# Optimization experiments

Hardware: AMD Instinct MI355X
Metric: run time of the kernel (lower is better)

## Reference

```python
import jax, jax.numpy as jnp
import numpy as np

DIM = 1024
NHEADS = 16
DIM_HEAD = 64
HIDDEN = NHEADS * DIM_HEAD  # 1024


def _xavier(key, fan_in, fan_out):
    limit = np.sqrt(6.0 / (fan_in + fan_out))
    return jax.random.uniform(key, (fan_in, fan_out), jnp.float32, -limit, limit)


def setup_inputs() -> dict:
    key = jax.random.key(0)
    kq, k1, k2, k3 = jax.random.split(key, 4)
    q = jax.random.normal(kq, (2, 2048, DIM), jnp.float32)
    Wq = _xavier(k1, DIM, HIDDEN)
    bq = jnp.zeros((HIDDEN,), jnp.float32)
    Wkv = _xavier(k2, DIM, 2 * HIDDEN)
    bkv = jnp.zeros((2 * HIDDEN,), jnp.float32)
    Wo = _xavier(k3, HIDDEN, DIM)
    bo = jnp.zeros((DIM,), jnp.float32)
    return {"q": q, "Wq": Wq, "bq": bq, "Wkv": Wkv, "bkv": bkv, "Wo": Wo, "bo": bo}


def reference(q, Wq, bq, Wkv, bkv, Wo, bo):
    scale = DIM_HEAD ** (-0.5)
    query = q @ Wq + bq                      # [b, s, hidden]
    kv = q @ Wkv + bkv                       # self-attention: kv from q
    key_, value = jnp.split(kv, 2, axis=-1)  # [b, s, hidden] each
    b, s, _ = query.shape
    query = query.reshape(b, s, NHEADS, DIM_HEAD)
    key_ = key_.reshape(b, s, NHEADS, DIM_HEAD)
    value = value.reshape(b, s, NHEADS, DIM_HEAD)
    scores = jnp.einsum('bqhd,bkhd->bhqk', query, key_) * scale
    attn = jax.nn.softmax(scores, axis=-1)
    out = jnp.einsum('bhqk,bkhd->bqhd', attn, value)
    out = out.reshape(b, s, HIDDEN)
    return out @ Wo + bo
```

## Files before the change

### kernel.cpp

```cpp
#include <hip/hip_runtime.h>

#define DIM 1024
#define NHEADS 16
#define DH 64
#define BATCH 2
#define SEQ 2048

typedef float f32x4 __attribute__((ext_vector_type(4)));
typedef short s16x8 __attribute__((ext_vector_type(8)));
typedef short s16x4 __attribute__((ext_vector_type(4)));

__device__ __forceinline__ short f2bf(float f) {
    union { float f; unsigned u; } v; v.f = f;
    unsigned r = v.u + 0x7fffu + ((v.u >> 16) & 1u);
    return (short)(r >> 16);
}

#if defined(__has_builtin)
#if __has_builtin(__builtin_amdgcn_cvt_pk_bf16_f32)
#define HAVE_PK_BF16 1
#endif
#endif
__device__ __forceinline__ unsigned f2bf_pk(float a, float b) {
#ifdef HAVE_PK_BF16
    typedef __bf16 bf16x2_t __attribute__((ext_vector_type(2)));
    bf16x2_t r = __builtin_amdgcn_cvt_pk_bf16_f32(a, b);
    return __builtin_bit_cast(unsigned, r);
#else
    return ((unsigned)(unsigned short)f2bf(b) << 16) | (unsigned short)f2bf(a);
#endif
}
__device__ __forceinline__ s16x4 pk4(float a, float b, float c, float d) {
    union { unsigned u[2]; s16x4 v; } x;
    x.u[0] = f2bf_pk(a, b); x.u[1] = f2bf_pk(c, d);
    return x.v;
}

#if defined(__has_builtin)
#if __has_builtin(__builtin_amdgcn_exp2f)
#define EXP2(x) __builtin_amdgcn_exp2f(x)
#endif
#endif
#ifndef EXP2
#define EXP2(x) exp2f(x)
#endif

#if defined(__has_builtin)
#if __has_builtin(__builtin_amdgcn_mfma_f32_16x16x16bf16_1k)
#define MFMA16(a, b, c) __builtin_amdgcn_mfma_f32_16x16x16bf16_1k(a, b, c, 0, 0, 0)
#elif __has_builtin(__builtin_amdgcn_mfma_f32_16x16x16_bf16)
#define MFMA16(a, b, c) __builtin_amdgcn_mfma_f32_16x16x16_bf16(a, b, c, 0, 0, 0)
#endif
#endif
#ifndef MFMA16
__device__ __forceinline__ f32x4 mfma16_asm(s16x4 a, s16x4 b, f32x4 c) {
    f32x4 d;
    asm volatile("v_mfma_f32_16x16x16_bf16 %0, %1, %2, %3"
                 : "=v"(d) : "v"(a), "v"(b), "0"(c));
    return d;
}
#define MFMA16(a, b, c) mfma16_asm(a, b, c)
#endif

__device__ __forceinline__ void gld16(const void* g, void* l) {
    __builtin_amdgcn_global_load_lds(
        (const __attribute__((address_space(1))) void*)g,
        (__attribute__((address_space(3))) void*)l, 16, 0, 0);
}

__global__ __launch_bounds__(256) void preproc_kernel(
    const float* __restrict__ q, short* __restrict__ qb,
    const float* __restrict__ Wq, const float* __restrict__ Wkv,
    const float* __restrict__ Wo, short* __restrict__ WT)
{
    const int bid = blockIdx.x;
    const int t = threadIdx.x;
    if (bid < 2048) {
        const int i = (bid * 256 + t) * 8;
        float4 a = *(const float4*)(q + i);
        float4 b = *(const float4*)(q + i + 4);
        union { unsigned u[4]; s16x8 v; } o;
        o.u[0] = f2bf_pk(a.x, a.y); o.u[1] = f2bf_pk(a.z, a.w);
        o.u[2] = f2bf_pk(b.x, b.y); o.u[3] = f2bf_pk(b.z, b.w);
        *(s16x8*)(qb + i) = o.v;
    } else {
        const int tb = bid - 2048;
        const int ng = (tb & 63) * 64 + (t & 63);
        const int k0 = ((tb >> 6) * 4 + (t >> 6)) * 8;
        const float* W; int n, N;
        if (ng < 1024)      { W = Wq;  n = ng;        N = 1024; }
        else if (ng < 3072) { W = Wkv; n = ng - 1024; N = 2048; }
        else                { W = Wo;  n = ng - 3072; N = 1024; }
        float v[8];
#pragma unroll
        for (int j = 0; j < 8; ++j) v[j] = W[(size_t)(k0 + j) * N + n];
        union { unsigned u[4]; s16x8 s; } o;
        o.u[0] = f2bf_pk(v[0], v[1]); o.u[1] = f2bf_pk(v[2], v[3]);
        o.u[2] = f2bf_pk(v[4], v[5]); o.u[3] = f2bf_pk(v[6], v[7]);
        *(s16x8*)&WT[(size_t)ng * 1024 + k0] = o.s;
    }
}

template<int TM, bool OUT_BF16>
__global__ __launch_bounds__(256) void gemm_mfma_kernel(
    const short* __restrict__ A, const short* __restrict__ Bt,
    const float* __restrict__ bias0, const float* __restrict__ bias1, int nsplit,
    float s0, float s1, void* __restrict__ C, short* __restrict__ VtG, int vt_split,
    int M, int N)
{
    const int K = 1024;
    constexpr int NI = (TM == 128) ? 4 : 2;
    __shared__ short As[TM * 32];
    __shared__ short Bs[128 * 32];

    const int t    = threadIdx.x;
    const int wave = t >> 6;
    const int lane = t & 63;
    const int col  = lane & 15;
    const int quad = lane >> 4;
    const int m0 = blockIdx.y * TM;
    const int n0 = blockIdx.x * 128;
    const int wroff = (TM == 128) ? (wave >> 1) * 64 : 0;
    const int wcoff = (TM == 128) ? (wave & 1) * 64 : wave * 32;

    f32x4 acc[4][NI];
#pragma unroll
    for (int mi = 0; mi < 4; ++mi)
#pragma unroll
        for (int ni = 0; ni < NI; ++ni) acc[mi][ni] = (f32x4){0.f, 0.f, 0.f, 0.f};

    constexpr int RPW = TM / 4;
    const int ldrowA = wave * RPW + (lane >> 2);
    const int ldrowB = wave * 32  + (lane >> 2);
    const int ldcol  = (lane & 3) * 8;
    const short* Ag = A  + (size_t)(m0 + ldrowA) * K + ldcol;
    const short* Bg = Bt + (size_t)(n0 + ldrowB) * K + ldcol;
    short* AsW = &As[wave * RPW * 32];
    short* BsW = &Bs[wave * 1024];

    for (int k0 = 0; k0 < K; k0 += 32) {
        __syncthreads();
        gld16(Ag + k0, AsW);
        if (TM == 128) gld16(Ag + 16 * K + k0, AsW + 512);
        gld16(Bg + k0,          BsW);
        gld16(Bg + 16 * K + k0, BsW + 512);
        __syncthreads();

        s16x8 aA[4], bB[NI];
#pragma unroll
        for (int mi = 0; mi < 4; ++mi)
            aA[mi] = *(const s16x8*)&As[(wroff + 16 * mi + col) * 32 + quad * 8];
#pragma unroll
        for (int ni = 0; ni < NI; ++ni)
            bB[ni] = *(const s16x8*)&Bs[(wcoff + 16 * ni + col) * 32 + quad * 8];
#pragma unroll
        for (int mi = 0; mi < 4; ++mi)
#pragma unroll
            for (int ni = 0; ni < NI; ++ni)
                acc[mi][ni] = __builtin_amdgcn_mfma_f32_16x16x32_bf16(aA[mi], bB[ni], acc[mi][ni], 0, 0, 0);
    }

    float bias_v[NI], scale_v[NI];
#pragma unroll
    for (int ni = 0; ni < NI; ++ni) {
        int nb = n0 + wcoff + 16 * ni + col;
        bias_v[ni]  = (nb < nsplit) ? bias0[nb] : bias1[nb - nsplit];
        scale_v[ni] = (nb < nsplit) ? s0 : s1;
    }

    if (vt_split >= 0 && n0 >= vt_split) {
#pragma unroll
        for (int mi = 0; mi < 4; ++mi)
#pragma unroll
            for (int ni = 0; ni < NI; ++ni) {
                const int gm = m0 + wroff + 16 * mi + quad * 4;
                const int gn = n0 + wcoff + 16 * ni + col;
                const int hv = (gn - vt_split) >> 6;
                const int dv = (gn - vt_split) & 63;
                const int bb = gm >> 11, tok = gm & 2047;
                f32x4 v;
#pragma unroll
                for (int r = 0; r < 4; ++r) v[r] = (acc[mi][ni][r] + bias_v[ni]) * scale_v[ni];
                *(s16x4*)(VtG + (size_t)((bb * NHEADS + hv) * 64 + dv) * SEQ + tok) =
                    pk4(v[0], v[1], v[2], v[3]);
            }
    } else {
#pragma unroll
        for (int mi = 0; mi < 4; ++mi)
#pragma unroll
            for (int ni = 0; ni < NI; ++ni)
#pragma unroll
                for (int r = 0; r < 4; ++r) {
                    const int gm = m0 + wroff + 16 * mi + quad * 4 + r;
                    const int gn = n0 + wcoff + 16 * ni + col;
                    float v = (acc[mi][ni][r] + bias_v[ni]) * scale_v[ni];
                    if (OUT_BF16) ((short*)C)[(size_t)gm * N + gn] = f2bf(v);
                    else          ((float*)C)[(size_t)gm * N + gn] = v;
                }
    }
}

__global__ __launch_bounds__(512) void attn_v7_kernel(
    const short* __restrict__ QKV,
    const short* __restrict__ VtG,
    short* __restrict__ O)
{
    const int qt = blockIdx.x;
    const int h  = blockIdx.y;
    const int b  = blockIdx.z;
    const int t  = threadIdx.x;
    const int wave = t >> 6;
    const int lane = t & 63;
    const int col  = lane & 15;
    const int quad = lane >> 4;
    const int wq = wave & 3;
    const int kh = wave >> 2;

    __shared__ short smem[4 * 64 * 72];

    const short* Qg = QKV + (size_t)(b * SEQ + qt * 256) * 3072 + h * DH;
    const short* Kg = QKV + (size_t)(b * SEQ) * 3072 + 1024 + h * DH;
    const short* VtRow = VtG + (size_t)(b * NHEADS + h) * 64 * SEQ;

    s16x8 aQ[4][2];
#pragma unroll
    for (int tq = 0; tq < 4; ++tq)
#pragma unroll
        for (int kq = 0; kq < 2; ++kq)
            aQ[tq][kq] = *(const s16x8*)(Qg + (size_t)(wq * 64 + 16 * tq + col) * 3072 + kq * 32 + quad * 8);

    f32x4 oa[4][4];
    float lsum[4] = {0.f, 0.f, 0.f, 0.f};
#pragma unroll
    for (int td = 0; td < 4; ++td)
#pragma unroll
        for (int tq = 0; tq < 4; ++tq) oa[td][tq] = (f32x4){0.f, 0.f, 0.f, 0.f};

    const int srow = t >> 3;
    const int sc8  = (t & 7) * 8;
    const short* KgS  = Kg + (size_t)srow * 3072 + sc8;
    const short* VtgS = VtRow + (size_t)srow * SEQ + sc8;
    s16x8 kx = *(const s16x8*)KgS;
    s16x8 vx = *(const s16x8*)VtgS;

    for (int kt = 0; kt < SEQ / 64; ++kt) {
        const int curK = (kt & 1) * 4608;
        const int curV = 9216 + (kt & 1) * 4608;
        *(s16x8*)&smem[curK + srow * 72 + sc8] = kx;
        *(s16x8*)&smem[curV + srow * 72 + sc8] = vx;
        {
            int nt = (kt + 1 < SEQ / 64) ? kt + 1 : kt;
            kx = *(const s16x8*)(KgS + (size_t)nt * 64 * 3072);
            vx = *(const s16x8*)(VtgS + (size_t)nt * 64);
        }
        __syncthreads();

        s16x8 aK[2][2];
#pragma unroll
        for (int tk = 0; tk < 2; ++tk)
#pragma unroll
            for (int kq = 0; kq < 2; ++kq)
                aK[tk][kq] = *(const s16x8*)&smem[curK + (kh * 32 + 16 * tk + col) * 72 + kq * 32 + quad * 8];

        s16x4 bP[2][4];
#pragma unroll
        for (int tk = 0; tk < 2; ++tk)
#pragma unroll
            for (int tq = 0; tq < 4; ++tq) {
                f32x4 a = (f32x4){0.f, 0.f, 0.f, 0.f};
                a = __builtin_amdgcn_mfma_f32_16x16x32_bf16(aK[tk][0], aQ[tq][0], a, 0, 0, 0);
                a = __builtin_amdgcn_mfma_f32_16x16x32_bf16(aK[tk][1], aQ[tq][1], a, 0, 0, 0);
                float p0 = EXP2(a[0]);
                float p1 = EXP2(a[1]);
                float p2 = EXP2(a[2]);
                float p3 = EXP2(a[3]);
                lsum[tq] += (p0 + p1) + (p2 + p3);
                bP[tk][tq] = pk4(p0, p1, p2, p3);
            }

#pragma unroll
        for (int td = 0; td < 4; ++td) {
            const int dv = 16 * td + col;
#pragma unroll
            for (int tk = 0; tk < 2; ++tk) {
                s16x4 aV = *(const s16x4*)&smem[curV + dv * 72 + kh * 32 + 16 * tk + quad * 4];
#pragma unroll
                for (int tq = 0; tq < 4; ++tq)
                    oa[td][tq] = MFMA16(aV, bP[tk][tq], oa[td][tq]);
            }
        }
    }

#pragma unroll
    for (int tq = 0; tq < 4; ++tq) {
        lsum[tq] += __shfl_xor(lsum[tq], 16);
        lsum[tq] += __shfl_xor(lsum[tq], 32);
    }

    __syncthreads();
    float* red  = (float*)smem;
    float* redl = red + 8192;
#pragma unroll
    for (int round = 0; round < 2; ++round) {
        if (wave >= 4 && ((wave >> 1) & 1) == round) {
            const int slot = wave & 1;
#pragma unroll
            for (int td = 0; td < 4; ++td)
#pragma unroll
                for (int tq = 0; tq < 4; ++tq)
#pragma unroll
                    for (int r = 0; r < 4; ++r)
                        red[slot * 4096 + (16 * td + quad * 4 + r) * 64 + 16 * tq + col] = oa[td][tq][r];
            if (quad == 0)
#pragma unroll
                for (int tq = 0; tq < 4; ++tq)
                    redl[slot * 64 + 16 * tq + col] = lsum[tq];
        }
        __syncthreads();
        if (wave < 4 && ((wave >> 1) & 1) == round) {
            const int slot = wave & 1;
#pragma unroll
            for (int td = 0; td < 4; ++td)
#pragma unroll
                for (int tq = 0; tq < 4; ++tq)
#pragma unroll
                    for (int r = 0; r < 4; ++r)
                        oa[td][tq][r] += red[slot * 4096 + (16 * td + quad * 4 + r) * 64 + 16 * tq + col];
#pragma unroll
            for (int tq = 0; tq < 4; ++tq)
                lsum[tq] += redl[slot * 64 + 16 * tq + col];
        }
        __syncthreads();
    }

    if (wave < 4) {
        short* Og = O + (size_t)(b * SEQ + qt * 256 + wq * 64) * DIM + h * DH;
        float inv[4];
#pragma unroll
        for (int tq = 0; tq < 4; ++tq) inv[tq] = 1.f / lsum[tq];
#pragma unroll
        for (int td = 0; td < 4; ++td)
#pragma unroll
            for (int tq = 0; tq < 4; ++tq)
                *(s16x4*)(Og + (size_t)(16 * tq + col) * DIM + 16 * td + quad * 4) =
                    pk4(oa[td][tq][0] * inv[tq], oa[td][tq][1] * inv[tq],
                        oa[td][tq][2] * inv[tq], oa[td][tq][3] * inv[tq]);
    }
}

extern "C" void kernel_launch(void* const* d_in, const int* in_sizes, int n_in,
                              void* d_out, int out_size, void* d_ws, size_t ws_size,
                              hipStream_t stream)
{
    const float* q   = (const float*)d_in[0];
    const float* Wq  = (const float*)d_in[1];
    const float* bq  = (const float*)d_in[2];
    const float* Wkv = (const float*)d_in[3];
    const float* bkv = (const float*)d_in[4];
    const float* Wo  = (const float*)d_in[5];
    const float* bo  = (const float*)d_in[6];
    float* out = (float*)d_out;

    const int M = BATCH * SEQ;

    short* qb     = (short*)d_ws;
    short* WT     = qb     + (size_t)M * DIM;
    short* QKVbuf = WT     + (size_t)4096 * DIM;
    short* AObuf  = QKVbuf + (size_t)M * 3 * DIM;
    short* VtG    = (short*)d_out;

    const float QSCALE = 0.18033688011112042f;

    preproc_kernel<<<4096, 256, 0, stream>>>(q, qb, Wq, Wkv, Wo, WT);

    gemm_mfma_kernel<128, true><<<dim3(3 * DIM / 128, M / 128), 256, 0, stream>>>(
        qb, WT, bq, bkv, DIM, QSCALE, 1.0f, QKVbuf, VtG, 2048, M, 3 * DIM);
    attn_v7_kernel<<<dim3(SEQ / 256, NHEADS, BATCH), 512, 0, stream>>>(QKVbuf, VtG, AObuf);
    gemm_mfma_kernel<64, false><<<dim3(DIM / 128, M / 64), 256, 0, stream>>>(
        AObuf, WT + (size_t)3072 * 1024, bo, bo, 1 << 30, 1.0f, 1.0f, out, nullptr, -1, M, DIM);
}
```

Before: 210.0 us.

## Move V transpose into a separate kernel and widen attention key tiles to 128

The QKV GEMM now writes V in its normal row layout, and a new kernel transposes V per head into VtG through shared memory. This replaces the strided 4-element scattered stores in the GEMM epilogue. The attention kernel now processes 128 keys per iteration instead of 64, with larger double-buffered K and Vt tiles in shared memory. That halves the number of barriers and loop iterations but raises LDS use, which may lower occupancy, and adds a kernel launch plus an extra pass over V in memory.

```diff
diff --git a/kernel.cpp b/kernel.cpp
--- a/kernel.cpp
+++ b/kernel.cpp
@@ -101,12 +101,37 @@
     }
 }
 
+__global__ __launch_bounds__(256) void transpose_v_kernel(
+    const short* __restrict__ QKV, short* __restrict__ VtG)
+{
+    const int t = threadIdx.x;
+    const int tok0 = blockIdx.x * 64;
+    const int h = blockIdx.y, b = blockIdx.z;
+    __shared__ short L[64 * 72];
+    const short* src = QKV + (size_t)(b * SEQ + tok0) * 3072 + 2048 + h * 64;
+#pragma unroll
+    for (int p = 0; p < 2; ++p) {
+        int r = p * 32 + (t >> 3);
+        *(s16x8*)&L[r * 72 + (t & 7) * 8] = *(const s16x8*)(src + (size_t)r * 3072 + (t & 7) * 8);
+    }
+    __syncthreads();
+    short* dst = VtG + (size_t)(b * NHEADS + h) * 64 * SEQ + tok0;
+#pragma unroll
+    for (int p = 0; p < 2; ++p) {
+        int u = p * 256 + t;
+        int dv = u >> 3, c = (u & 7) * 8;
+        s16x8 o;
+#pragma unroll
+        for (int j = 0; j < 8; ++j) o[j] = L[(c + j) * 72 + dv];
+        *(s16x8*)(dst + (size_t)dv * SEQ + c) = o;
+    }
+}
+
 template<int TM, bool OUT_BF16>
 __global__ __launch_bounds__(256) void gemm_mfma_kernel(
     const short* __restrict__ A, const short* __restrict__ Bt,
     const float* __restrict__ bias0, const float* __restrict__ bias1, int nsplit,
-    float s0, float s1, void* __restrict__ C, short* __restrict__ VtG, int vt_split,
-    int M, int N)
+    float s0, float s1, void* __restrict__ C, int M, int N)
 {
     const int K = 1024;
     constexpr int NI = (TM == 128) ? 4 : 2;
@@ -168,39 +193,21 @@
         scale_v[ni] = (nb < nsplit) ? s0 : s1;
     }
 
-    if (vt_split >= 0 && n0 >= vt_split) {
-#pragma unroll
-        for (int mi = 0; mi < 4; ++mi)
-#pragma unroll
-            for (int ni = 0; ni < NI; ++ni) {
-                const int gm = m0 + wroff + 16 * mi + quad * 4;
+#pragma unroll
+    for (int mi = 0; mi < 4; ++mi)
+#pragma unroll
+        for (int ni = 0; ni < NI; ++ni)
+#pragma unroll
+            for (int r = 0; r < 4; ++r) {
+                const int gm = m0 + wroff + 16 * mi + quad * 4 + r;
                 const int gn = n0 + wcoff + 16 * ni + col;
-                const int hv = (gn - vt_split) >> 6;
-                const int dv = (gn - vt_split) & 63;
-                const int bb = gm >> 11, tok = gm & 2047;
-                f32x4 v;
-#pragma unroll
-                for (int r = 0; r < 4; ++r) v[r] = (acc[mi][ni][r] + bias_v[ni]) * scale_v[ni];
-                *(s16x4*)(VtG + (size_t)((bb * NHEADS + hv) * 64 + dv) * SEQ + tok) =
-                    pk4(v[0], v[1], v[2], v[3]);
+                float v = (acc[mi][ni][r] + bias_v[ni]) * scale_v[ni];
+                if (OUT_BF16) ((short*)C)[(size_t)gm * N + gn] = f2bf(v);
+                else          ((float*)C)[(size_t)gm * N + gn] = v;
             }
-    } else {
-#pragma unroll
-        for (int mi = 0; mi < 4; ++mi)
-#pragma unroll
-            for (int ni = 0; ni < NI; ++ni)
-#pragma unroll
-                for (int r = 0; r < 4; ++r) {
-                    const int gm = m0 + wroff + 16 * mi + quad * 4 + r;
-                    const int gn = n0 + wcoff + 16 * ni + col;
-                    float v = (acc[mi][ni][r] + bias_v[ni]) * scale_v[ni];
-                    if (OUT_BF16) ((short*)C)[(size_t)gm * N + gn] = f2bf(v);
-                    else          ((float*)C)[(size_t)gm * N + gn] = v;
-                }
-    }
-}
-
-__global__ __launch_bounds__(512) void attn_v7_kernel(
+}
+
+__global__ __launch_bounds__(512) void attn_v8_kernel(
     const short* __restrict__ QKV,
     const short* __restrict__ VtG,
     short* __restrict__ O)
@@ -216,7 +223,7 @@
     const int wq = wave & 3;
     const int kh = wave >> 2;
 
-    __shared__ short smem[4 * 64 * 72];
+    __shared__ short smem[35840];
 
     const short* Qg = QKV + (size_t)(b * SEQ + qt * 256) * 3072 + h * DH;
     const short* Kg = QKV + (size_t)(b * SEQ) * 3072 + 1024 + h * DH;
@@ -238,55 +245,61 @@
 
     const int srow = t >> 3;
     const int sc8  = (t & 7) * 8;
+    const int dvS  = t >> 4;
+    const int tokc = (t & 15) * 8;
     const short* KgS  = Kg + (size_t)srow * 3072 + sc8;
-    const short* VtgS = VtRow + (size_t)srow * SEQ + sc8;
-    s16x8 kx = *(const s16x8*)KgS;
-    s16x8 vx = *(const s16x8*)VtgS;
-
-    for (int kt = 0; kt < SEQ / 64; ++kt) {
-        const int curK = (kt & 1) * 4608;
-        const int curV = 9216 + (kt & 1) * 4608;
-        *(s16x8*)&smem[curK + srow * 72 + sc8] = kx;
-        *(s16x8*)&smem[curV + srow * 72 + sc8] = vx;
+    const short* VtgS = VtRow + (size_t)dvS * SEQ + tokc;
+
+    s16x8 kx[2], vx[2];
+#pragma unroll
+    for (int p = 0; p < 2; ++p) {
+        kx[p] = *(const s16x8*)(KgS + (size_t)p * 64 * 3072);
+        vx[p] = *(const s16x8*)(VtgS + (size_t)p * 32 * SEQ);
+    }
+
+    for (int kt = 0; kt < SEQ / 128; ++kt) {
+        const int KsOff = (kt & 1) * 9216;
+        const int VtOff = 18432 + (kt & 1) * 8704;
+#pragma unroll
+        for (int p = 0; p < 2; ++p) {
+            *(s16x8*)&smem[KsOff + (srow + p * 64) * 72 + sc8] = kx[p];
+            *(s16x8*)&smem[VtOff + (dvS + p * 32) * 136 + tokc] = vx[p];
+        }
         {
-            int nt = (kt + 1 < SEQ / 64) ? kt + 1 : kt;
-            kx = *(const s16x8*)(KgS + (size_t)nt * 64 * 3072);
-            vx = *(const s16x8*)(VtgS + (size_t)nt * 64);
-        }
-        __syncthreads();
-
-        s16x8 aK[2][2];
-#pragma unroll
-        for (int tk = 0; tk < 2; ++tk)
-#pragma unroll
-            for (int kq = 0; kq < 2; ++kq)
-                aK[tk][kq] = *(const s16x8*)&smem[curK + (kh * 32 + 16 * tk + col) * 72 + kq * 32 + quad * 8];
-
-        s16x4 bP[2][4];
-#pragma unroll
-        for (int tk = 0; tk < 2; ++tk)
+            int nt = (kt + 1 < SEQ / 128) ? kt + 1 : kt;
+#pragma unroll
+            for (int p = 0; p < 2; ++p) {
+                kx[p] = *(const s16x8*)(KgS + (size_t)(nt * 128 + p * 64) * 3072);
+                vx[p] = *(const s16x8*)(VtgS + (size_t)p * 32 * SEQ + nt * 128);
+            }
+        }
+        __syncthreads();
+
+#pragma unroll
+        for (int tk = 0; tk < 4; ++tk) {
+            const int krow = kh * 64 + 16 * tk + col;
+            s16x8 aK0 = *(const s16x8*)&smem[KsOff + krow * 72 + quad * 8];
+            s16x8 aK1 = *(const s16x8*)&smem[KsOff + krow * 72 + 32 + quad * 8];
+
+            s16x4 bP[4];
 #pragma unroll
             for (int tq = 0; tq < 4; ++tq) {
                 f32x4 a = (f32x4){0.f, 0.f, 0.f, 0.f};
-                a = __builtin_amdgcn_mfma_f32_16x16x32_bf16(aK[tk][0], aQ[tq][0], a, 0, 0, 0);
-                a = __builtin_amdgcn_mfma_f32_16x16x32_bf16(aK[tk][1], aQ[tq][1], a, 0, 0, 0);
+                a = __builtin_amdgcn_mfma_f32_16x16x32_bf16(aK0, aQ[tq][0], a, 0, 0, 0);
+                a = __builtin_amdgcn_mfma_f32_16x16x32_bf16(aK1, aQ[tq][1], a, 0, 0, 0);
                 float p0 = EXP2(a[0]);
                 float p1 = EXP2(a[1]);
                 float p2 = EXP2(a[2]);
                 float p3 = EXP2(a[3]);
                 lsum[tq] += (p0 + p1) + (p2 + p3);
-                bP[tk][tq] = pk4(p0, p1, p2, p3);
+                bP[tq] = pk4(p0, p1, p2, p3);
             }
-
-#pragma unroll
-        for (int td = 0; td < 4; ++td) {
-            const int dv = 16 * td + col;
-#pragma unroll
-            for (int tk = 0; tk < 2; ++tk) {
-                s16x4 aV = *(const s16x4*)&smem[curV + dv * 72 + kh * 32 + 16 * tk + quad * 4];
+#pragma unroll
+            for (int td = 0; td < 4; ++td) {
+                s16x4 aV = *(const s16x4*)&smem[VtOff + (16 * td + col) * 136 + kh * 64 + 16 * tk + quad * 4];
 #pragma unroll
                 for (int tq = 0; tq < 4; ++tq)
-                    oa[td][tq] = MFMA16(aV, bP[tk][tq], oa[td][tq]);
+                    oa[td][tq] = MFMA16(aV, bP[tq], oa[td][tq]);
             }
         }
     }
@@ -374,8 +387,9 @@
     preproc_kernel<<<4096, 256, 0, stream>>>(q, qb, Wq, Wkv, Wo, WT);
 
     gemm_mfma_kernel<128, true><<<dim3(3 * DIM / 128, M / 128), 256, 0, stream>>>(
-        qb, WT, bq, bkv, DIM, QSCALE, 1.0f, QKVbuf, VtG, 2048, M, 3 * DIM);
-    attn_v7_kernel<<<dim3(SEQ / 256, NHEADS, BATCH), 512, 0, stream>>>(QKVbuf, VtG, AObuf);
+        qb, WT, bq, bkv, DIM, QSCALE, 1.0f, QKVbuf, M, 3 * DIM);
+    transpose_v_kernel<<<dim3(SEQ / 64, NHEADS, BATCH), 256, 0, stream>>>(QKVbuf, VtG);
+    attn_v8_kernel<<<dim3(SEQ / 256, NHEADS, BATCH), 512, 0, stream>>>(QKVbuf, VtG, AObuf);
     gemm_mfma_kernel<64, false><<<dim3(DIM / 128, M / 64), 256, 0, stream>>>(
-        AObuf, WT + (size_t)3072 * 1024, bo, bo, 1 << 30, 1.0f, 1.0f, out, nullptr, -1, M, DIM);
-}
+        AObuf, WT + (size_t)3072 * 1024, bo, bo, 1 << 30, 1.0f, 1.0f, out, M, DIM);
+}
```

Result: no change. 208.5 us (-0.7%).
